# Optimization experiments

Measured on AMD Instinct MI355X. Metric: run time of the kernel, lower is better.

## Reference

```python
import jax, jax.numpy as jnp
import numpy as np

N_NODES = 100000
N_EDGES = 1600000
IN_DIM = 300
HID = 128
N_CLASSES = 3
N_ASPECTS = 2048


def setup_inputs() -> dict:
    key = jax.random.key(0)
    ks = jax.random.split(key, 8)
    features = jax.random.normal(ks[0], (N_NODES, IN_DIM), dtype=jnp.float32)
    edge_index = jax.random.randint(ks[1], (2, N_EDGES), 0, N_NODES, dtype=jnp.int64)
    aspect_indices = jax.random.randint(ks[2], (N_ASPECTS,), 0, N_NODES, dtype=jnp.int64)
    W1 = jax.random.normal(ks[3], (IN_DIM, HID), dtype=jnp.float32) * (1.0 / np.sqrt(IN_DIM))
    b1 = jnp.zeros((HID,), dtype=jnp.float32)
    W2 = jax.random.normal(ks[4], (HID, HID), dtype=jnp.float32) * (1.0 / np.sqrt(HID))
    b2 = jnp.zeros((HID,), dtype=jnp.float32)
    Wc = jax.random.normal(ks[5], (HID, N_CLASSES), dtype=jnp.float32) * (1.0 / np.sqrt(HID))
    bc = jnp.zeros((N_CLASSES,), dtype=jnp.float32)
    return {"features": features, "edge_index": edge_index, "aspect_indices": aspect_indices,
            "W1": W1, "b1": b1, "W2": W2, "b2": b2, "Wc": Wc, "bc": bc}


def _gcn_norm(edge_index, num_nodes):
    # PyG GCNConv: add self-loops, symmetric normalization D^-1/2 (A+I) D^-1/2
    loop = jnp.arange(num_nodes, dtype=edge_index.dtype)
    src = jnp.concatenate([edge_index[0], loop])
    dst = jnp.concatenate([edge_index[1], loop])
    deg = jax.ops.segment_sum(jnp.ones_like(dst, dtype=jnp.float32), dst,
                              num_segments=num_nodes)
    deg_inv_sqrt = jnp.where(deg > 0, jax.lax.rsqrt(deg), 0.0)
    norm = deg_inv_sqrt[src] * deg_inv_sqrt[dst]  # [E + N]
    return src, dst, norm


def _gcn_conv(x, src, dst, norm, W, b, num_nodes):
    h = x @ W                            # transform first (dim reduction)
    msg = h[src] * norm[:, None]         # gather + scale  [E+N, HID]
    out = jax.ops.segment_sum(msg, dst, num_segments=num_nodes)  # scatter-add
    return out + b


def reference(features, edge_index, aspect_indices, W1, b1, W2, b2, Wc, bc):
    num_nodes = features.shape[0]
    src, dst, norm = _gcn_norm(edge_index, num_nodes)
    h = _gcn_conv(features, src, dst, norm, W1, b1, num_nodes)
    h = jax.nn.relu(h)
    # dropout(p=0.3) -> identity in eval mode
    h = _gcn_conv(h, src, dst, norm, W2, b2, num_nodes)
    aspect_embeddings = h[aspect_indices]          # [N_ASPECTS, HID]
    logits = aspect_embeddings @ Wc + bc           # [N_ASPECTS, 3]
    return logits
```

## Files before the change

kernel.cpp:

```cpp
#include <hip/hip_runtime.h>

constexpr int NN = 100000;
constexpr int NE = 1600000;
constexpr int IN_DIM = 300;
constexpr int HID = 128;
constexpr int NA = 2048;
constexpr int NF_CAP = 50000;

using short8 = __attribute__((ext_vector_type(8))) short;
using f32x4  = __attribute__((ext_vector_type(4))) float;

__device__ inline unsigned short f2bf(float x) {
    unsigned u = __float_as_uint(x);
    unsigned r = u + 0x7FFFu + ((u >> 16) & 1u);
    return (unsigned short)(r >> 16);
}
__device__ inline float bf2f(unsigned short h) {
    return __uint_as_float(((unsigned)h) << 16);
}

__device__ inline void gload_lds16(const void* g, void* l) {
    __builtin_amdgcn_global_load_lds(
        (const __attribute__((address_space(1))) unsigned int*)g,
        (__attribute__((address_space(3))) unsigned int*)l, 16, 0, 0);
}

__global__ void k_flag2(const int* __restrict__ asp, unsigned char* __restrict__ flags2,
                        int* __restrict__ flags1) {
    int i = blockIdx.x * blockDim.x + threadIdx.x;
    if (i < NA) {
        int n = asp[i];
        flags2[n] = 1;
        flags1[n] = 1;
    }
}

__global__ void k_deg_mark(const int* __restrict__ src, const int* __restrict__ dst,
                           const unsigned char* __restrict__ flags2,
                           int* __restrict__ degi, int* __restrict__ flags1) {
    int e = blockIdx.x * blockDim.x + threadIdx.x;
    if (e < NE) {
        int d = dst[e];
        atomicAdd(&degi[d], 1);
        if (flags2[d]) flags1[src[e]] = 1;
    }
}

__global__ void k_dis(const int* __restrict__ degi, float* __restrict__ dis) {
    int i = blockIdx.x * blockDim.x + threadIdx.x;
    if (i < NN) dis[i] = rsqrtf((float)degi[i] + 1.0f);
}

__global__ __launch_bounds__(1024) void k_scan2_local(const int* __restrict__ degi,
                                                      const int* __restrict__ flags1,
                                                      int* __restrict__ off,
                                                      int* __restrict__ off2,
                                                      int* __restrict__ blksum,
                                                      int* __restrict__ blksum2) {
    __shared__ int sh[1024];
    __shared__ int sh2[1024];
    int t = threadIdx.x;
    int base = blockIdx.x * 1024;
    int ok = (base + t < NN);
    int f = ok ? flags1[base + t] : 0;
    int v = f ? degi[base + t] : 0;
    sh[t] = v;
    sh2[t] = f;
    __syncthreads();
    for (int s = 1; s < 1024; s <<= 1) {
        int a = (t >= s) ? sh[t - s] : 0;
        int a2 = (t >= s) ? sh2[t - s] : 0;
        __syncthreads();
        sh[t] += a;
        sh2[t] += a2;
        __syncthreads();
    }
    if (ok) {
        off[base + t] = sh[t] - v;
        off2[base + t] = sh2[t] - f;
    }
    if (t == 1023) {
        blksum[blockIdx.x] = sh[1023];
        blksum2[blockIdx.x] = sh2[1023];
    }
}

__global__ __launch_bounds__(128) void k_scan2_blk(int* __restrict__ blksum,
                                                   int* __restrict__ blksum2, int nb) {
    __shared__ int sh[128];
    __shared__ int sh2[128];
    int t = threadIdx.x;
    int v = (t < nb) ? blksum[t] : 0;
    int v2 = (t < nb) ? blksum2[t] : 0;
    sh[t] = v;
    sh2[t] = v2;
    __syncthreads();
    for (int s = 1; s < 128; s <<= 1) {
        int a = (t >= s) ? sh[t - s] : 0;
        int a2 = (t >= s) ? sh2[t - s] : 0;
        __syncthreads();
        sh[t] += a;
        sh2[t] += a2;
        __syncthreads();
    }
    if (t < nb) {
        blksum[t] = sh[t] - v;
        blksum2[t] = sh2[t] - v2;
    }
}

__global__ void k_scan2_add(int* __restrict__ off, int* __restrict__ off2,
                            const int* __restrict__ blksum, const int* __restrict__ blksum2) {
    int i = blockIdx.x * blockDim.x + threadIdx.x;
    if (i < NN) {
        off[i] += blksum[i >> 10];
        off2[i] += blksum2[i >> 10];
    }
}

__global__ void k_fill(const int* __restrict__ src, const int* __restrict__ dst,
                       const int* __restrict__ flags1,
                       int* __restrict__ off, int* __restrict__ csr) {
    int e = blockIdx.x * blockDim.x + threadIdx.x;
    if (e < NE) {
        int d = dst[e];
        if (flags1[d]) {
            int pos = atomicAdd(&off[d], 1);
            csr[pos] = src[e];
        }
    }
}

__global__ void k_compact(const int* __restrict__ flags1, const int* __restrict__ off2,
                          int* __restrict__ list, int* __restrict__ remap, int* __restrict__ nf) {
    int i = blockIdx.x * blockDim.x + threadIdx.x;
    if (i < NN && flags1[i]) {
        int p = off2[i];
        if (p < NF_CAP) { list[p] = i; remap[i] = p; }
    }
    if (i == NN - 1) {
        int tot = off2[i] + flags1[i];
        *nf = (tot < NF_CAP) ? tot : NF_CAP;
    }
}

__global__ void k_prepB(const float* __restrict__ B, unsigned short* __restrict__ img,
                        int K, int NT) {
    int i = blockIdx.x * blockDim.x + threadIdx.x;
    if (i >= NT * 4096) return;
    int kt = i >> 12;
    int rem = i & 4095;
    int ct = rem >> 9;
    int s = rem & 511;
    int lg = s >> 7;
    int lr = (s >> 3) & 15;
    int j = s & 7;
    int k = kt * 32 + lg * 8 + j;
    int col = ct * 16 + lr;
    float v = (k < K) ? B[k * 128 + col] : 0.f;
    unsigned short hi = f2bf(v);
    unsigned short lo = f2bf(v - bf2f(hi));
    img[kt * 8192 + ct * 1024 + s] = hi;
    img[kt * 8192 + ct * 1024 + 512 + s] = lo;
}

template <int K, int NT>
__global__ __launch_bounds__(512, 4) void k_gemm_mfma(const float* __restrict__ A,
        const unsigned short* __restrict__ Bimg,
        float* __restrict__ C, int M, const int* __restrict__ Mptr) {
    const int Mv = Mptr ? *Mptr : M;
    const int row0 = blockIdx.x * 128;
    if (row0 >= Mv) return;
    __shared__ alignas(16) unsigned short ldsB[2][8192];
    const int t = threadIdx.x;
    const int w = t >> 6;
    const int l = t & 63;
    const int lr = l & 15;
    const int lg = l >> 4;

    const int r0 = row0 + w * 16 + lr;
    const long a0 = (long)(r0 < Mv ? r0 : Mv - 1) * K + lg * 8;

    f32x4 acc[8];
#pragma unroll
    for (int ct = 0; ct < 8; ++ct) acc[ct] = (f32x4){0.f, 0.f, 0.f, 0.f};

    float4 A0[2], A1[2];

    auto LOADA = [&](float4* buf, int kt) {
        const int k0 = kt * 32 + lg * 8;
        const float* s0 = A + a0 + kt * 32;
        if (k0 + 8 <= K) {
            buf[0] = *(const float4*)(s0);
            buf[1] = *(const float4*)(s0 + 4);
        } else {
            float t0[8];
#pragma unroll
            for (int j = 0; j < 8; ++j) t0[j] = (k0 + j < K) ? s0[j] : 0.f;
            buf[0] = make_float4(t0[0], t0[1], t0[2], t0[3]);
            buf[1] = make_float4(t0[4], t0[5], t0[6], t0[7]);
        }
    };

    auto STAGE_B = [&](int buf, int kt) {
        const char* g = (const char*)Bimg + (long)kt * 16384 + w * 2048 + l * 16;
        gload_lds16(g, &ldsB[buf][w * 1024]);
        gload_lds16(g + 1024, &ldsB[buf][w * 1024 + 512]);
    };

    auto CONV = [&](const float4* buf, short8& h0, short8& e0) {
        float v0[8] = {buf[0].x, buf[0].y, buf[0].z, buf[0].w, buf[1].x, buf[1].y, buf[1].z, buf[1].w};
#pragma unroll
        for (int j = 0; j < 8; ++j) {
            unsigned short hi = f2bf(v0[j]);
            h0[j] = (short)hi;
            e0[j] = (short)f2bf(v0[j] - bf2f(hi));
        }
    };

    auto COMPUTE = [&](const unsigned short* bbuf, short8 ah, short8 al) {
#pragma unroll
        for (int ct = 0; ct < 8; ++ct) {
            const unsigned short* bp = bbuf + ct * 1024 + lg * 128 + lr * 8;
            short8 bh = *(const short8*)(bp);
            short8 bl = *(const short8*)(bp + 512);
            acc[ct] = __builtin_amdgcn_mfma_f32_16x16x32_bf16(ah, bh, acc[ct], 0, 0, 0);
            acc[ct] = __builtin_amdgcn_mfma_f32_16x16x32_bf16(al, bh, acc[ct], 0, 0, 0);
            acc[ct] = __builtin_amdgcn_mfma_f32_16x16x32_bf16(ah, bl, acc[ct], 0, 0, 0);
        }
    };

    LOADA(A0, 0);
    STAGE_B(0, 0);
    __syncthreads();
    for (int kt = 0; kt < NT; kt += 2) {
        if (kt + 1 < NT) {
            LOADA(A1, kt + 1);
            STAGE_B(1, kt + 1);
        }
        {
            short8 h0, e0;
            CONV(A0, h0, e0);
            COMPUTE(ldsB[0], h0, e0);
        }
        __syncthreads();
        if (kt + 1 < NT) {
            if (kt + 2 < NT) {
                LOADA(A0, kt + 2);
                STAGE_B(0, kt + 2);
            }
            short8 h0, e0;
            CONV(A1, h0, e0);
            COMPUTE(ldsB[1], h0, e0);
            __syncthreads();
        }
    }
#pragma unroll
    for (int ct = 0; ct < 8; ++ct)
#pragma unroll
        for (int r = 0; r < 4; ++r) {
            int row = row0 + w * 16 + lg * 4 + r;
            if (row < Mv) C[(long)row * 128 + ct * 16 + lr] = acc[ct][r];
        }
}

__global__ __launch_bounds__(256) void k_gather1(const int* __restrict__ list,
                                                 const int* __restrict__ nf,
                                                 const int* __restrict__ csr,
                                                 const int* __restrict__ offpost,
                                                 const float* __restrict__ dis,
                                                 const float* __restrict__ h1,
                                                 const float* __restrict__ b1,
                                                 float* __restrict__ out) {
    int wave = threadIdx.x >> 6;
    int lane = threadIdx.x & 63;
    int half = lane >> 5;
    int sl = lane & 31;
    int idx = blockIdx.x * 4 + wave;
    if (idx >= *nf) return;
    int n = list[idx];
    int start = (n == 0) ? 0 : offpost[n - 1];
    int end = offpost[n];
    float dn = dis[n];
    float ax = 0.f, ay = 0.f, az = 0.f, aw = 0.f;
    int i = start + half;
    for (; i + 2 < end; i += 4) {
        int s0 = csr[i], s1 = csr[i + 2];
        float w0 = dis[s0], w1 = dis[s1];
        float4 v0 = *(const float4*)&h1[(long)s0 * HID + sl * 4];
        float4 v1 = *(const float4*)&h1[(long)s1 * HID + sl * 4];
        ax += w0 * v0.x + w1 * v1.x;
        ay += w0 * v0.y + w1 * v1.y;
        az += w0 * v0.z + w1 * v1.z;
        aw += w0 * v0.w + w1 * v1.w;
    }
    if (i < end) {
        int s = csr[i];
        float wgt = dis[s];
        float4 v = *(const float4*)&h1[(long)s * HID + sl * 4];
        ax += wgt * v.x;
        ay += wgt * v.y;
        az += wgt * v.z;
        aw += wgt * v.w;
    }
    ax += __shfl_xor(ax, 32);
    ay += __shfl_xor(ay, 32);
    az += __shfl_xor(az, 32);
    aw += __shfl_xor(aw, 32);
    if (half == 0) {
        float4 hv = *(const float4*)&h1[(long)n * HID + sl * 4];
        float4 bv = *(const float4*)&b1[sl * 4];
        float4 r;
        r.x = fmaxf(dn * (ax + dn * hv.x) + bv.x, 0.f);
        r.y = fmaxf(dn * (ay + dn * hv.y) + bv.y, 0.f);
        r.z = fmaxf(dn * (az + dn * hv.z) + bv.z, 0.f);
        r.w = fmaxf(dn * (aw + dn * hv.w) + bv.w, 0.f);
        *reinterpret_cast<float4*>(&out[(long)idx * HID + sl * 4]) = r;
    }
}

__global__ __launch_bounds__(256) void k_gather2(const int* __restrict__ asp,
                                                 const int* __restrict__ remap,
                                                 const int* __restrict__ csr,
                                                 const int* __restrict__ offpost,
                                                 const float* __restrict__ dis,
                                                 const float* __restrict__ t2,
                                                 const float* __restrict__ b2,
                                                 const float* __restrict__ Wc,
                                                 const float* __restrict__ bc,
                                                 float* __restrict__ out) {
    int wave = threadIdx.x >> 6;
    int lane = threadIdx.x & 63;
    int a = blockIdx.x * 4 + wave;
    if (a >= NA) return;
    int n = asp[a];
    int start = (n == 0) ? 0 : offpost[n - 1];
    int end = offpost[n];
    float dn = dis[n];
    float ax = 0.f, ay = 0.f;
    int i = start;
    for (; i + 4 <= end; i += 4) {
        int s0 = csr[i], s1 = csr[i + 1], s2 = csr[i + 2], s3 = csr[i + 3];
        float w0 = dis[s0], w1 = dis[s1], w2 = dis[s2], w3 = dis[s3];
        int r0 = remap[s0], r1 = remap[s1], r2 = remap[s2], r3 = remap[s3];
        float2 v0 = *(const float2*)&t2[(long)r0 * HID + lane * 2];
        float2 v1 = *(const float2*)&t2[(long)r1 * HID + lane * 2];
        float2 v2 = *(const float2*)&t2[(long)r2 * HID + lane * 2];
        float2 v3 = *(const float2*)&t2[(long)r3 * HID + lane * 2];
        ax += w0 * v0.x + w1 * v1.x + w2 * v2.x + w3 * v3.x;
        ay += w0 * v0.y + w1 * v1.y + w2 * v2.y + w3 * v3.y;
    }
    for (; i < end; ++i) {
        int s = csr[i];
        float w = dis[s];
        float2 v = *(const float2*)&t2[(long)remap[s] * HID + lane * 2];
        ax += w * v.x;
        ay += w * v.y;
    }
    float2 hv = *(const float2*)&t2[(long)remap[n] * HID + lane * 2];
    float vx = dn * (ax + dn * hv.x) + b2[2 * lane];
    float vy = dn * (ay + dn * hv.y) + b2[2 * lane + 1];
    float l0 = vx * Wc[(2 * lane) * 3 + 0] + vy * Wc[(2 * lane + 1) * 3 + 0];
    float l1 = vx * Wc[(2 * lane) * 3 + 1] + vy * Wc[(2 * lane + 1) * 3 + 1];
    float l2 = vx * Wc[(2 * lane) * 3 + 2] + vy * Wc[(2 * lane + 1) * 3 + 2];
#pragma unroll
    for (int s = 32; s > 0; s >>= 1) {
        l0 += __shfl_xor(l0, s);
        l1 += __shfl_xor(l1, s);
        l2 += __shfl_xor(l2, s);
    }
    if (lane == 0) {
        out[a * 3 + 0] = l0 + bc[0];
        out[a * 3 + 1] = l1 + bc[1];
        out[a * 3 + 2] = l2 + bc[2];
    }
}

extern "C" void kernel_launch(void* const* d_in, const int* in_sizes, int n_in,
                              void* d_out, int out_size, void* d_ws, size_t ws_size,
                              hipStream_t stream) {
    const float* features = (const float*)d_in[0];
    const int* ei = (const int*)d_in[1];
    const int* src = ei;
    const int* dst = ei + NE;
    const int* asp = (const int*)d_in[2];
    const float* W1 = (const float*)d_in[3];
    const float* b1 = (const float*)d_in[4];
    const float* W2 = (const float*)d_in[5];
    const float* b2 = (const float*)d_in[6];
    const float* Wc = (const float*)d_in[7];
    const float* bc = (const float*)d_in[8];
    float* out = (float*)d_out;

    char* ws = (char*)d_ws;
    float* dis   = (float*)(ws + 0);
    int*   degi  = (int*)  (ws + 400384);
    unsigned short* bimg1 = (unsigned short*)(ws + 400384);
    unsigned short* bimg2 = (unsigned short*)(ws + 400384 + 163840);
    int*   off   = (int*)  (ws + 800768);
    int*   blksum  = (int*)(ws + 1201152);
    int*   blksum2 = (int*)(ws + 1202176);
    int*   nf    = (int*)  (ws + 1203200);
    int*   csr   = (int*)  (ws + 1203328);
    int*   flags1= (int*)  (ws + 7603328);
    int*   off2  = (int*)  (ws + 8003328);
    int*   list  = (int*)  (ws + 8403328);
    int*   remap = (int*)  (ws + 8803328);
    float* bufA  = (float*)(ws + 9203328);
    float* bufB  = (float*)(ws + 60403328);
    unsigned char* flags2 = (unsigned char*)(ws + 86003328);

    const int NB = (NN + 1023) / 1024;

    hipMemsetAsync(degi, 0, NN * sizeof(int), stream);
    hipMemsetAsync(flags1, 0, NN * sizeof(int), stream);
    hipMemsetAsync(flags2, 0, NN, stream);
    k_flag2<<<(NA + 255) / 256, 256, 0, stream>>>(asp, flags2, flags1);
    k_deg_mark<<<(NE + 255) / 256, 256, 0, stream>>>(src, dst, flags2, degi, flags1);
    k_dis<<<(NN + 255) / 256, 256, 0, stream>>>(degi, dis);

    k_scan2_local<<<NB, 1024, 0, stream>>>(degi, flags1, off, off2, blksum, blksum2);
    k_scan2_blk<<<1, 128, 0, stream>>>(blksum, blksum2, NB);
    k_scan2_add<<<(NN + 255) / 256, 256, 0, stream>>>(off, off2, blksum, blksum2);

    k_prepB<<<(10 * 4096 + 255) / 256, 256, 0, stream>>>(W1, bimg1, IN_DIM, 10);
    k_prepB<<<(4 * 4096 + 255) / 256, 256, 0, stream>>>(W2, bimg2, HID, 4);

    k_compact<<<(NN + 255) / 256, 256, 0, stream>>>(flags1, off2, list, remap, nf);
    k_fill<<<(NE + 255) / 256, 256, 0, stream>>>(src, dst, flags1, off, csr);

    k_gemm_mfma<IN_DIM, 10><<<(NN + 127) / 128, 512, 0, stream>>>(features, bimg1, bufA, NN, nullptr);
    k_gather1<<<(NF_CAP + 3) / 4, 256, 0, stream>>>(list, nf, csr, off, dis, bufA, b1, bufB);

    k_gemm_mfma<HID, 4><<<(NF_CAP + 127) / 128, 512, 0, stream>>>(bufB, bimg2, bufA, 0, nf);
    k_gather2<<<(NA + 3) / 4, 256, 0, stream>>>(asp, remap, csr, off, dis, bufA, b2, Wc, bc, out);
}
```

Baseline: 228.2 us.

## Co-schedule GEMM1 halves with edge passes and fold small kernels into scan

The first feature GEMM is split into two halves. Each half is launched in the same grid as one of the edge passes: degree counting plus neighbour marking, then CSR fill. This lets MFMA blocks and atomic-heavy edge blocks share the GPU instead of running back to back. The rsqrt degree normalisation now happens inside the local scan, and list/remap compaction inside the scan-add kernel, which removes several launches and a few passes over the node arrays. The degree buffer moves into the later bufB region so it no longer aliases the weight images, which are now prepared earlier. The cost is larger fused grids with mixed block types, which can reduce occupancy for the GEMM blocks.

```diff
diff --git a/kernel.cpp b/kernel.cpp
--- a/kernel.cpp
+++ b/kernel.cpp
@@ -6,6 +6,8 @@
 constexpr int HID = 128;
 constexpr int NA = 2048;
 constexpr int NF_CAP = 50000;
+constexpr int G1_BLOCKS = 391;
+constexpr int EDGE_BLOCKS = 3125;
 
 using short8 = __attribute__((ext_vector_type(8))) short;
 using f32x4  = __attribute__((ext_vector_type(4))) float;
@@ -35,35 +37,22 @@
     }
 }
 
-__global__ void k_deg_mark(const int* __restrict__ src, const int* __restrict__ dst,
-                           const unsigned char* __restrict__ flags2,
-                           int* __restrict__ degi, int* __restrict__ flags1) {
-    int e = blockIdx.x * blockDim.x + threadIdx.x;
-    if (e < NE) {
-        int d = dst[e];
-        atomicAdd(&degi[d], 1);
-        if (flags2[d]) flags1[src[e]] = 1;
-    }
-}
-
-__global__ void k_dis(const int* __restrict__ degi, float* __restrict__ dis) {
-    int i = blockIdx.x * blockDim.x + threadIdx.x;
-    if (i < NN) dis[i] = rsqrtf((float)degi[i] + 1.0f);
-}
-
 __global__ __launch_bounds__(1024) void k_scan2_local(const int* __restrict__ degi,
                                                       const int* __restrict__ flags1,
                                                       int* __restrict__ off,
                                                       int* __restrict__ off2,
                                                       int* __restrict__ blksum,
-                                                      int* __restrict__ blksum2) {
+                                                      int* __restrict__ blksum2,
+                                                      float* __restrict__ dis) {
     __shared__ int sh[1024];
     __shared__ int sh2[1024];
     int t = threadIdx.x;
     int base = blockIdx.x * 1024;
     int ok = (base + t < NN);
     int f = ok ? flags1[base + t] : 0;
-    int v = f ? degi[base + t] : 0;
+    int d = ok ? degi[base + t] : 0;
+    int v = f ? d : 0;
+    if (ok) dis[base + t] = rsqrtf((float)d + 1.0f);
     sh[t] = v;
     sh2[t] = f;
     __syncthreads();
@@ -110,37 +99,24 @@
 }
 
 __global__ void k_scan2_add(int* __restrict__ off, int* __restrict__ off2,
-                            const int* __restrict__ blksum, const int* __restrict__ blksum2) {
+                            const int* __restrict__ blksum, const int* __restrict__ blksum2,
+                            const int* __restrict__ flags1,
+                            int* __restrict__ list, int* __restrict__ remap,
+                            int* __restrict__ nf) {
     int i = blockIdx.x * blockDim.x + threadIdx.x;
     if (i < NN) {
         off[i] += blksum[i >> 10];
-        off2[i] += blksum2[i >> 10];
-    }
-}
-
-__global__ void k_fill(const int* __restrict__ src, const int* __restrict__ dst,
-                       const int* __restrict__ flags1,
-                       int* __restrict__ off, int* __restrict__ csr) {
-    int e = blockIdx.x * blockDim.x + threadIdx.x;
-    if (e < NE) {
-        int d = dst[e];
-        if (flags1[d]) {
-            int pos = atomicAdd(&off[d], 1);
-            csr[pos] = src[e];
-        }
-    }
-}
-
-__global__ void k_compact(const int* __restrict__ flags1, const int* __restrict__ off2,
-                          int* __restrict__ list, int* __restrict__ remap, int* __restrict__ nf) {
-    int i = blockIdx.x * blockDim.x + threadIdx.x;
-    if (i < NN && flags1[i]) {
-        int p = off2[i];
-        if (p < NF_CAP) { list[p] = i; remap[i] = p; }
-    }
-    if (i == NN - 1) {
-        int tot = off2[i] + flags1[i];
-        *nf = (tot < NF_CAP) ? tot : NF_CAP;
+        int o2 = off2[i] + blksum2[i >> 10];
+        off2[i] = o2;
+        int f = flags1[i];
+        if (f && o2 < NF_CAP) {
+            list[o2] = i;
+            remap[i] = o2;
+        }
+        if (i == NN - 1) {
+            int tot = o2 + f;
+            *nf = (tot < NF_CAP) ? tot : NF_CAP;
+        }
     }
 }
 
@@ -165,13 +141,13 @@
 }
 
 template <int K, int NT>
-__global__ __launch_bounds__(512, 4) void k_gemm_mfma(const float* __restrict__ A,
+__device__ __forceinline__ void gemm_dev(int gbid, const float* __restrict__ A,
         const unsigned short* __restrict__ Bimg,
         float* __restrict__ C, int M, const int* __restrict__ Mptr) {
+    __shared__ alignas(16) unsigned short ldsB[2][8192];
     const int Mv = Mptr ? *Mptr : M;
-    const int row0 = blockIdx.x * 128;
+    const int row0 = gbid * 128;
     if (row0 >= Mv) return;
-    __shared__ alignas(16) unsigned short ldsB[2][8192];
     const int t = threadIdx.x;
     const int w = t >> 6;
     const int l = t & 63;
@@ -262,6 +238,48 @@
             int row = row0 + w * 16 + lg * 4 + r;
             if (row < Mv) C[(long)row * 128 + ct * 16 + lr] = acc[ct][r];
         }
+}
+
+__global__ __launch_bounds__(512, 4) void k_fusedA(const float* __restrict__ A,
+        const unsigned short* __restrict__ Bimg, float* __restrict__ C,
+        const int* __restrict__ src, const int* __restrict__ dst,
+        const unsigned char* __restrict__ flags2,
+        int* __restrict__ degi, int* __restrict__ flags1) {
+    if (blockIdx.x < G1_BLOCKS) {
+        gemm_dev<IN_DIM, 10>(blockIdx.x, A, Bimg, C, NN, nullptr);
+    } else {
+        int e = (blockIdx.x - G1_BLOCKS) * 512 + threadIdx.x;
+        if (e < NE) {
+            int d = dst[e];
+            atomicAdd(&degi[d], 1);
+            if (flags2[d]) flags1[src[e]] = 1;
+        }
+    }
+}
+
+__global__ __launch_bounds__(512, 4) void k_fusedB(const float* __restrict__ A,
+        const unsigned short* __restrict__ Bimg, float* __restrict__ C,
+        const int* __restrict__ src, const int* __restrict__ dst,
+        const int* __restrict__ flags1,
+        int* __restrict__ off, int* __restrict__ csr) {
+    if (blockIdx.x < G1_BLOCKS) {
+        gemm_dev<IN_DIM, 10>(blockIdx.x + G1_BLOCKS, A, Bimg, C, NN, nullptr);
+    } else {
+        int e = (blockIdx.x - G1_BLOCKS) * 512 + threadIdx.x;
+        if (e < NE) {
+            int d = dst[e];
+            if (flags1[d]) {
+                int pos = atomicAdd(&off[d], 1);
+                csr[pos] = src[e];
+            }
+        }
+    }
+}
+
+__global__ __launch_bounds__(512, 4) void k_gemm2(const float* __restrict__ A,
+        const unsigned short* __restrict__ Bimg, float* __restrict__ C,
+        const int* __restrict__ nf) {
+    gemm_dev<HID, 4>(blockIdx.x, A, Bimg, C, 0, nf);
 }
 
 __global__ __launch_bounds__(256) void k_gather1(const int* __restrict__ list,
@@ -394,7 +412,6 @@
 
     char* ws = (char*)d_ws;
     float* dis   = (float*)(ws + 0);
-    int*   degi  = (int*)  (ws + 400384);
     unsigned short* bimg1 = (unsigned short*)(ws + 400384);
     unsigned short* bimg2 = (unsigned short*)(ws + 400384 + 163840);
     int*   off   = (int*)  (ws + 800768);
@@ -408,6 +425,7 @@
     int*   remap = (int*)  (ws + 8803328);
     float* bufA  = (float*)(ws + 9203328);
     float* bufB  = (float*)(ws + 60403328);
+    int*   degi  = (int*)  (ws + 60403328);
     unsigned char* flags2 = (unsigned char*)(ws + 86003328);
 
     const int NB = (NN + 1023) / 1024;
@@ -416,22 +434,22 @@
     hipMemsetAsync(flags1, 0, NN * sizeof(int), stream);
     hipMemsetAsync(flags2, 0, NN, stream);
     k_flag2<<<(NA + 255) / 256, 256, 0, stream>>>(asp, flags2, flags1);
-    k_deg_mark<<<(NE + 255) / 256, 256, 0, stream>>>(src, dst, flags2, degi, flags1);
-    k_dis<<<(NN + 255) / 256, 256, 0, stream>>>(degi, dis);
-
-    k_scan2_local<<<NB, 1024, 0, stream>>>(degi, flags1, off, off2, blksum, blksum2);
-    k_scan2_blk<<<1, 128, 0, stream>>>(blksum, blksum2, NB);
-    k_scan2_add<<<(NN + 255) / 256, 256, 0, stream>>>(off, off2, blksum, blksum2);
-
     k_prepB<<<(10 * 4096 + 255) / 256, 256, 0, stream>>>(W1, bimg1, IN_DIM, 10);
     k_prepB<<<(4 * 4096 + 255) / 256, 256, 0, stream>>>(W2, bimg2, HID, 4);
 
-    k_compact<<<(NN + 255) / 256, 256, 0, stream>>>(flags1, off2, list, remap, nf);
-    k_fill<<<(NE + 255) / 256, 256, 0, stream>>>(src, dst, flags1, off, csr);
-
-    k_gemm_mfma<IN_DIM, 10><<<(NN + 127) / 128, 512, 0, stream>>>(features, bimg1, bufA, NN, nullptr);
+    k_fusedA<<<G1_BLOCKS + EDGE_BLOCKS, 512, 0, stream>>>(
+        features, bimg1, bufA, src, dst, flags2, degi, flags1);
+
+    k_scan2_local<<<NB, 1024, 0, stream>>>(degi, flags1, off, off2, blksum, blksum2, dis);
+    k_scan2_blk<<<1, 128, 0, stream>>>(blksum, blksum2, NB);
+    k_scan2_add<<<(NN + 255) / 256, 256, 0, stream>>>(off, off2, blksum, blksum2,
+                                                      flags1, list, remap, nf);
+
+    k_fusedB<<<G1_BLOCKS + EDGE_BLOCKS, 512, 0, stream>>>(
+        features, bimg1, bufA, src, dst, flags1, off, csr);
+
     k_gather1<<<(NF_CAP + 3) / 4, 256, 0, stream>>>(list, nf, csr, off, dis, bufA, b1, bufB);
 
-    k_gemm_mfma<HID, 4><<<(NF_CAP + 127) / 128, 512, 0, stream>>>(bufB, bimg2, bufA, 0, nf);
+    k_gemm2<<<(NF_CAP + 127) / 128, 512, 0, stream>>>(bufB, bimg2, bufA, nf);
     k_gather2<<<(NA + 3) / 4, 256, 0, stream>>>(asp, remap, csr, off, dis, bufA, b2, Wc, bc, out);
 }
```

After: 199.6 us. 1.14x faster.
